# Kernel optimization log

Measured on AMD Instinct MI355X. Metric: run time of the kernel, lower is better.

The kernel has to match this reference:

```python
import jax, jax.numpy as jnp
import numpy as np

MAT_MODE = [(0, 1), (0, 2), (1, 2)]
VEC_MODE = [2, 1, 0]


def _sample_plane(plane, gx, gy):
    """Bilinear grid_sample, align_corners=True, border clamp.
    plane: [C,H,W]; gx,gy in [-1,1], shape [N]; grid x->W, y->H. Returns [C,N]."""
    C, H, W = plane.shape
    ix = (gx + 1.0) * 0.5 * (W - 1)
    iy = (gy + 1.0) * 0.5 * (H - 1)
    ix0f = jnp.clip(jnp.floor(ix), 0, W - 1)
    iy0f = jnp.clip(jnp.floor(iy), 0, H - 1)
    ix0 = ix0f.astype(jnp.int32)
    iy0 = iy0f.astype(jnp.int32)
    ix1 = jnp.minimum(ix0 + 1, W - 1)
    iy1 = jnp.minimum(iy0 + 1, H - 1)
    wx = ix - ix0f  # [N]
    wy = iy - iy0f
    v00 = plane[:, iy0, ix0]  # [C,N]
    v01 = plane[:, iy0, ix1]
    v10 = plane[:, iy1, ix0]
    v11 = plane[:, iy1, ix1]
    top = v00 + wx * (v01 - v00)
    bot = v10 + wx * (v11 - v10)
    return top + wy * (bot - top)


def _sample_line(line, gz):
    """1D linear interp (grid_sample on [C,G,1] with grid (0,z)). line: [C,G]. Returns [C,N]."""
    C, G = line.shape
    iz = (gz + 1.0) * 0.5 * (G - 1)
    iz0f = jnp.clip(jnp.floor(iz), 0, G - 1)
    iz0 = iz0f.astype(jnp.int32)
    iz1 = jnp.minimum(iz0 + 1, G - 1)
    wz = iz - iz0f
    v0 = line[:, iz0]
    v1 = line[:, iz1]
    return v0 + wz * (v1 - v0)


def setup_inputs() -> dict:
    key = jax.random.key(0)
    ks = jax.random.split(key, 7)
    N, C, G = 524288, 48, 512
    scale = 0.1 ** 0.5
    xyz = jax.random.uniform(ks[0], (N, 3), dtype=jnp.float32, minval=-1.0, maxval=1.0)
    planes = [scale * jax.random.normal(ks[1 + i], (C, G, G), dtype=jnp.float32) for i in range(3)]
    lines = [scale * jax.random.normal(ks[4 + i], (C, G), dtype=jnp.float32) for i in range(3)]
    return {"xyz": xyz,
            "plane0": planes[0], "plane1": planes[1], "plane2": planes[2],
            "line0": lines[0], "line1": lines[1], "line2": lines[2]}


def reference(xyz, plane0, plane1, plane2, line0, line1, line2):
    planes = (plane0, plane1, plane2)
    lines = (line0, line1, line2)
    feats = []
    for i in range(3):
        m0, m1 = MAT_MODE[i]
        pc = _sample_plane(planes[i], xyz[:, m0], xyz[:, m1])   # [C,N]
        lc = _sample_line(lines[i], xyz[:, VEC_MODE[i]])          # [C,N]
        feats.append(pc * lc)
    return tuple(feats)
```

## Files before the change

kernel.cpp:

```cpp
#include <hip/hip_runtime.h>
#include <hip/hip_fp16.h>

#define GSZ 512
#define CCH 48
#define GG (GSZ*GSZ)

__global__ __launch_bounds__(256) void transpose_plane(const float* __restrict__ in,
                                                       __half* __restrict__ out) {
    __shared__ float tile[CCH][65];
    const int t = threadIdx.x;
    const int pos0 = blockIdx.x * 64;
    #pragma unroll
    for (int k = 0; k < 12; ++k) {
        int e = k * 256 + t;
        int c = e >> 6;
        int p = e & 63;
        tile[c][p] = in[c * GG + pos0 + p];
    }
    __syncthreads();
    #pragma unroll
    for (int k = 0; k < 6; ++k) {
        int e = (k * 256 + t) * 2;
        int p = e / 48;
        int c = e - p * 48;
        __half2 h;
        h.x = __float2half(tile[c][p]);
        h.y = __float2half(tile[c + 1][p]);
        *((__half2*)(out + (size_t)pos0 * CCH + e)) = h;
    }
}

__global__ __launch_bounds__(256) void transpose_lines(
    const float* __restrict__ i0, const float* __restrict__ i1, const float* __restrict__ i2,
    __half* __restrict__ o0, __half* __restrict__ o1, __half* __restrict__ o2) {
    int idx = blockIdx.x * blockDim.x + threadIdx.x;
    const int total = CCH * GSZ;
    if (idx >= 3 * total) return;
    int w = idx / total;
    int r = idx - w * total;
    int c = r / GSZ;
    int p = r - c * GSZ;
    const float* in = (w == 0) ? i0 : (w == 1) ? i1 : i2;
    __half* out = (w == 0) ? o0 : (w == 1) ? o1 : o2;
    out[p * CCH + c] = __float2half(in[c * GSZ + p]);
}

union H8 { int4 v; __half h[8]; };

__global__ __launch_bounds__(256) void gather_fused(
    const float* __restrict__ xyz,
    const __half* __restrict__ p0, const __half* __restrict__ p1, const __half* __restrict__ p2,
    const __half* __restrict__ l0, const __half* __restrict__ l1, const __half* __restrict__ l2,
    float* __restrict__ out, int N) {
    int n = blockIdx.x * blockDim.x + threadIdx.x;
    if (n >= N) return;
    float x = xyz[3 * n + 0], y = xyz[3 * n + 1], z = xyz[3 * n + 2];

    float gx[3] = {x, x, y};
    float gy[3] = {y, z, z};
    float gz[3] = {z, y, x};

    int   po[3][4];
    int   lo[3][2];
    float wx[3], wy[3], wz[3];
    #pragma unroll
    for (int i = 0; i < 3; ++i) {
        float ix = (gx[i] + 1.0f) * 0.5f * (float)(GSZ - 1);
        float iy = (gy[i] + 1.0f) * 0.5f * (float)(GSZ - 1);
        float ix0f = fminf(fmaxf(floorf(ix), 0.0f), (float)(GSZ - 1));
        float iy0f = fminf(fmaxf(floorf(iy), 0.0f), (float)(GSZ - 1));
        int ix0 = (int)ix0f, iy0 = (int)iy0f;
        int ix1 = min(ix0 + 1, GSZ - 1);
        int iy1 = min(iy0 + 1, GSZ - 1);
        wx[i] = ix - ix0f;
        wy[i] = iy - iy0f;
        po[i][0] = (iy0 * GSZ + ix0) * CCH;
        po[i][1] = (iy0 * GSZ + ix1) * CCH;
        po[i][2] = (iy1 * GSZ + ix0) * CCH;
        po[i][3] = (iy1 * GSZ + ix1) * CCH;
        float iz = (gz[i] + 1.0f) * 0.5f * (float)(GSZ - 1);
        float iz0f = fminf(fmaxf(floorf(iz), 0.0f), (float)(GSZ - 1));
        int iz0 = (int)iz0f;
        int iz1 = min(iz0 + 1, GSZ - 1);
        wz[i] = iz - iz0f;
        lo[i][0] = iz0 * CCH;
        lo[i][1] = iz1 * CCH;
    }

    const size_t CN = (size_t)CCH * (size_t)N;
    #pragma unroll
    for (int i = 0; i < 3; ++i) {
        const __half* pp = (i == 0) ? p0 : (i == 1) ? p1 : p2;
        const __half* ll = (i == 0) ? l0 : (i == 1) ? l1 : l2;
        float* op = out + (size_t)i * CN + n;
        #pragma unroll
        for (int cc = 0; cc < CCH; cc += 8) {
            H8 a00, a01, a10, a11, b0, b1;
            a00.v = *(const int4*)(pp + po[i][0] + cc);
            a01.v = *(const int4*)(pp + po[i][1] + cc);
            a10.v = *(const int4*)(pp + po[i][2] + cc);
            a11.v = *(const int4*)(pp + po[i][3] + cc);
            b0.v  = *(const int4*)(ll + lo[i][0] + cc);
            b1.v  = *(const int4*)(ll + lo[i][1] + cc);
            #pragma unroll
            for (int j = 0; j < 8; ++j) {
                float v00 = __half2float(a00.h[j]);
                float v01 = __half2float(a01.h[j]);
                float v10 = __half2float(a10.h[j]);
                float v11 = __half2float(a11.h[j]);
                float top = fmaf(wx[i], v01 - v00, v00);
                float bot = fmaf(wx[i], v11 - v10, v10);
                float pc  = fmaf(wy[i], bot - top, top);
                float lv0 = __half2float(b0.h[j]);
                float lv1 = __half2float(b1.h[j]);
                float lc  = fmaf(wz[i], lv1 - lv0, lv0);
                op[(size_t)(cc + j) * N] = pc * lc;
            }
        }
    }
}

__global__ __launch_bounds__(256) void gather_direct(
    const float* __restrict__ xyz,
    const float* __restrict__ p0, const float* __restrict__ p1, const float* __restrict__ p2,
    const float* __restrict__ l0, const float* __restrict__ l1, const float* __restrict__ l2,
    float* __restrict__ out, int N) {
    int n = blockIdx.x * blockDim.x + threadIdx.x;
    if (n >= N) return;
    float x = xyz[3 * n + 0], y = xyz[3 * n + 1], z = xyz[3 * n + 2];
    float gx[3] = {x, x, y};
    float gy[3] = {y, z, z};
    float gz[3] = {z, y, x};
    int q[3][4], lz[3][2];
    float wx[3], wy[3], wz[3];
    #pragma unroll
    for (int i = 0; i < 3; ++i) {
        float ix = (gx[i] + 1.0f) * 0.5f * (float)(GSZ - 1);
        float iy = (gy[i] + 1.0f) * 0.5f * (float)(GSZ - 1);
        float ix0f = fminf(fmaxf(floorf(ix), 0.0f), (float)(GSZ - 1));
        float iy0f = fminf(fmaxf(floorf(iy), 0.0f), (float)(GSZ - 1));
        int ix0 = (int)ix0f, iy0 = (int)iy0f;
        int ix1 = min(ix0 + 1, GSZ - 1);
        int iy1 = min(iy0 + 1, GSZ - 1);
        wx[i] = ix - ix0f;
        wy[i] = iy - iy0f;
        q[i][0] = iy0 * GSZ + ix0;
        q[i][1] = iy0 * GSZ + ix1;
        q[i][2] = iy1 * GSZ + ix0;
        q[i][3] = iy1 * GSZ + ix1;
        float iz = (gz[i] + 1.0f) * 0.5f * (float)(GSZ - 1);
        float iz0f = fminf(fmaxf(floorf(iz), 0.0f), (float)(GSZ - 1));
        int iz0 = (int)iz0f;
        int iz1 = min(iz0 + 1, GSZ - 1);
        wz[i] = iz - iz0f;
        lz[i][0] = iz0;
        lz[i][1] = iz1;
    }
    const size_t CN = (size_t)CCH * (size_t)N;
    for (int c = 0; c < CCH; ++c) {
        #pragma unroll
        for (int i = 0; i < 3; ++i) {
            const float* pp = (i == 0) ? p0 : (i == 1) ? p1 : p2;
            const float* ll = (i == 0) ? l0 : (i == 1) ? l1 : l2;
            const float* pc_ = pp + (size_t)c * GG;
            float v00 = pc_[q[i][0]];
            float v01 = pc_[q[i][1]];
            float v10 = pc_[q[i][2]];
            float v11 = pc_[q[i][3]];
            float top = fmaf(wx[i], v01 - v00, v00);
            float bot = fmaf(wx[i], v11 - v10, v10);
            float pcv = fmaf(wy[i], bot - top, top);
            float lv0 = ll[c * GSZ + lz[i][0]];
            float lv1 = ll[c * GSZ + lz[i][1]];
            float lc  = fmaf(wz[i], lv1 - lv0, lv0);
            out[(size_t)i * CN + (size_t)c * N + n] = pcv * lc;
        }
    }
}

extern "C" void kernel_launch(void* const* d_in, const int* in_sizes, int n_in,
                              void* d_out, int out_size, void* d_ws, size_t ws_size,
                              hipStream_t stream) {
    const float* xyz = (const float*)d_in[0];
    const float* pl0 = (const float*)d_in[1];
    const float* pl1 = (const float*)d_in[2];
    const float* pl2 = (const float*)d_in[3];
    const float* ln0 = (const float*)d_in[4];
    const float* ln1 = (const float*)d_in[5];
    const float* ln2 = (const float*)d_in[6];
    float* out = (float*)d_out;
    const int N = in_sizes[0] / 3;

    const size_t planeElems = (size_t)GG * CCH;
    const size_t lineElems  = (size_t)GSZ * CCH;
    const size_t need = (3 * planeElems + 3 * lineElems) * sizeof(__half);

    if (ws_size >= need) {
        __half* wp0 = (__half*)d_ws;
        __half* wp1 = wp0 + planeElems;
        __half* wp2 = wp1 + planeElems;
        __half* wl0 = wp2 + planeElems;
        __half* wl1 = wl0 + lineElems;
        __half* wl2 = wl1 + lineElems;

        transpose_plane<<<GG / 64, 256, 0, stream>>>(pl0, wp0);
        transpose_plane<<<GG / 64, 256, 0, stream>>>(pl1, wp1);
        transpose_plane<<<GG / 64, 256, 0, stream>>>(pl2, wp2);
        transpose_lines<<<(3 * CCH * GSZ + 255) / 256, 256, 0, stream>>>(
            ln0, ln1, ln2, wl0, wl1, wl2);
        gather_fused<<<(N + 255) / 256, 256, 0, stream>>>(
            xyz, wp0, wp1, wp2, wl0, wl1, wl2, out, N);
    } else {
        gather_direct<<<(N + 255) / 256, 256, 0, stream>>>(
            xyz, pl0, pl1, pl2, ln0, ln1, ln2, out, N);
    }
}
```

Measured before the change: 941.1 us.

## Morton-sort query points before gathering to improve plane cache locality

Adds a counting sort of query points into a 32^3 Morton-ordered grid (histogram, single-block scan, atomic scatter). The gather then runs on the sorted points so neighbouring threads hit nearby plane texels, and writes fp16 features into a point-major buffer. A separate permute kernel restores the original order and writes the fp32 channel-major output. The three plane transposes are also merged into one launch. This adds four kernels, a memset and an extra fp16 round-trip of the features, and it only runs when the workspace is large enough.

```diff
diff --git a/kernel.cpp b/kernel.cpp
--- a/kernel.cpp
+++ b/kernel.cpp
@@ -4,9 +4,15 @@
 #define GSZ 512
 #define CCH 48
 #define GG (GSZ*GSZ)
-
-__global__ __launch_bounds__(256) void transpose_plane(const float* __restrict__ in,
-                                                       __half* __restrict__ out) {
+#define CBITS 5
+#define CDIM (1 << CBITS)
+#define CELLS (CDIM * CDIM * CDIM)
+
+__global__ __launch_bounds__(256) void transpose_planes3(
+    const float* __restrict__ i0, const float* __restrict__ i1, const float* __restrict__ i2,
+    __half* __restrict__ o0, __half* __restrict__ o1, __half* __restrict__ o2) {
+    const float* in = (blockIdx.y == 0) ? i0 : (blockIdx.y == 1) ? i1 : i2;
+    __half* out     = (blockIdx.y == 0) ? o0 : (blockIdx.y == 1) ? o1 : o2;
     __shared__ float tile[CCH][65];
     const int t = threadIdx.x;
     const int pos0 = blockIdx.x * 64;
@@ -45,23 +51,83 @@
     out[p * CCH + c] = __float2half(in[c * GSZ + p]);
 }
 
+__device__ __forceinline__ unsigned spread5(unsigned a) {
+    a &= 31u;
+    a = (a | (a << 8)) & 0x100Fu;
+    a = (a | (a << 4)) & 0x10C3u;
+    a = (a | (a << 2)) & 0x1249u;
+    return a;
+}
+__device__ __forceinline__ unsigned cell_of(float x, float y, float z) {
+    const float s = 0.5f * (float)CDIM;
+    unsigned cx = (unsigned)fminf(fmaxf((x + 1.0f) * s, 0.0f), (float)(CDIM - 1));
+    unsigned cy = (unsigned)fminf(fmaxf((y + 1.0f) * s, 0.0f), (float)(CDIM - 1));
+    unsigned cz = (unsigned)fminf(fmaxf((z + 1.0f) * s, 0.0f), (float)(CDIM - 1));
+    return spread5(cx) | (spread5(cy) << 1) | (spread5(cz) << 2);
+}
+
+__global__ __launch_bounds__(256) void hist_k(const float* __restrict__ xyz,
+                                              unsigned* __restrict__ hist, int N) {
+    int n = blockIdx.x * 256 + threadIdx.x;
+    if (n >= N) return;
+    float x = xyz[3 * n], y = xyz[3 * n + 1], z = xyz[3 * n + 2];
+    atomicAdd(&hist[cell_of(x, y, z)], 1u);
+}
+
+__global__ __launch_bounds__(1024) void scan_k(unsigned* __restrict__ h) {
+    __shared__ unsigned partials[1024];
+    const int t = threadIdx.x;
+    unsigned loc[CELLS / 1024];
+    unsigned s = 0;
+    #pragma unroll
+    for (int j = 0; j < CELLS / 1024; ++j) { loc[j] = h[t * (CELLS / 1024) + j]; s += loc[j]; }
+    partials[t] = s;
+    __syncthreads();
+    for (int off = 1; off < 1024; off <<= 1) {
+        unsigned v = (t >= off) ? partials[t - off] : 0u;
+        __syncthreads();
+        partials[t] += v;
+        __syncthreads();
+    }
+    unsigned running = (t > 0) ? partials[t - 1] : 0u;
+    #pragma unroll
+    for (int j = 0; j < CELLS / 1024; ++j) {
+        unsigned c = loc[j];
+        h[t * (CELLS / 1024) + j] = running;
+        running += c;
+    }
+}
+
+__global__ __launch_bounds__(256) void scatter_k(const float* __restrict__ xyz,
+                                                 unsigned* __restrict__ offs,
+                                                 unsigned* __restrict__ invPerm,
+                                                 float4* __restrict__ sxyz, int N) {
+    int n = blockIdx.x * 256 + threadIdx.x;
+    if (n >= N) return;
+    float x = xyz[3 * n], y = xyz[3 * n + 1], z = xyz[3 * n + 2];
+    unsigned p = atomicAdd(&offs[cell_of(x, y, z)], 1u);
+    invPerm[n] = p;
+    sxyz[p] = make_float4(x, y, z, 0.0f);
+}
+
 union H8 { int4 v; __half h[8]; };
 
-__global__ __launch_bounds__(256) void gather_fused(
-    const float* __restrict__ xyz,
+__global__ __launch_bounds__(256) void gather_sorted(
+    const float4* __restrict__ sxyz,
     const __half* __restrict__ p0, const __half* __restrict__ p1, const __half* __restrict__ p2,
     const __half* __restrict__ l0, const __half* __restrict__ l1, const __half* __restrict__ l2,
-    float* __restrict__ out, int N) {
-    int n = blockIdx.x * blockDim.x + threadIdx.x;
-    if (n >= N) return;
-    float x = xyz[3 * n + 0], y = xyz[3 * n + 1], z = xyz[3 * n + 2];
+    __half* __restrict__ feats, int N) {
+    int b = blockIdx.x, nb = gridDim.x;
+    int chunk = ((nb & 7) == 0) ? ((b & 7) * (nb >> 3) + (b >> 3)) : b;
+    int p = chunk * 256 + threadIdx.x;
+    if (p >= N) return;
+    float4 q = sxyz[p];
+    float x = q.x, y = q.y, z = q.z;
 
     float gx[3] = {x, x, y};
     float gy[3] = {y, z, z};
     float gz[3] = {z, y, x};
-
-    int   po[3][4];
-    int   lo[3][2];
+    int po[3][4], lo[3][2];
     float wx[3], wy[3], wz[3];
     #pragma unroll
     for (int i = 0; i < 3; ++i) {
@@ -87,6 +153,96 @@
         lo[i][1] = iz1 * CCH;
     }
 
+    __half* fb = feats + (size_t)p * 144;
+    #pragma unroll
+    for (int i = 0; i < 3; ++i) {
+        const __half* pp = (i == 0) ? p0 : (i == 1) ? p1 : p2;
+        const __half* ll = (i == 0) ? l0 : (i == 1) ? l1 : l2;
+        #pragma unroll
+        for (int cc = 0; cc < CCH; cc += 8) {
+            H8 a00, a01, a10, a11, b0, b1, r;
+            a00.v = *(const int4*)(pp + po[i][0] + cc);
+            a01.v = *(const int4*)(pp + po[i][1] + cc);
+            a10.v = *(const int4*)(pp + po[i][2] + cc);
+            a11.v = *(const int4*)(pp + po[i][3] + cc);
+            b0.v  = *(const int4*)(ll + lo[i][0] + cc);
+            b1.v  = *(const int4*)(ll + lo[i][1] + cc);
+            #pragma unroll
+            for (int j = 0; j < 8; ++j) {
+                float v00 = __half2float(a00.h[j]);
+                float v01 = __half2float(a01.h[j]);
+                float v10 = __half2float(a10.h[j]);
+                float v11 = __half2float(a11.h[j]);
+                float top = fmaf(wx[i], v01 - v00, v00);
+                float bot = fmaf(wx[i], v11 - v10, v10);
+                float pc  = fmaf(wy[i], bot - top, top);
+                float lv0 = __half2float(b0.h[j]);
+                float lv1 = __half2float(b1.h[j]);
+                float lc  = fmaf(wz[i], lv1 - lv0, lv0);
+                r.h[j] = __float2half(pc * lc);
+            }
+            *(int4*)(fb + i * 48 + cc) = r.v;
+        }
+    }
+}
+
+__global__ __launch_bounds__(256) void permute_k(
+    const unsigned* __restrict__ invPerm, const __half* __restrict__ feats,
+    float* __restrict__ out, int N) {
+    int n = blockIdx.x * 256 + threadIdx.x;
+    if (n >= N) return;
+    const __half* fb = feats + (size_t)invPerm[n] * 144;
+    const size_t CN = (size_t)CCH * (size_t)N;
+    #pragma unroll
+    for (int i = 0; i < 3; ++i) {
+        H8 v[6];
+        #pragma unroll
+        for (int k = 0; k < 6; ++k) v[k].v = *(const int4*)(fb + i * 48 + k * 8);
+        float* op = out + (size_t)i * CN + n;
+        #pragma unroll
+        for (int k = 0; k < 6; ++k)
+            #pragma unroll
+            for (int j = 0; j < 8; ++j)
+                op[(size_t)(k * 8 + j) * N] = __half2float(v[k].h[j]);
+    }
+}
+
+__global__ __launch_bounds__(256) void gather_fused(
+    const float* __restrict__ xyz,
+    const __half* __restrict__ p0, const __half* __restrict__ p1, const __half* __restrict__ p2,
+    const __half* __restrict__ l0, const __half* __restrict__ l1, const __half* __restrict__ l2,
+    float* __restrict__ out, int N) {
+    int n = blockIdx.x * 256 + threadIdx.x;
+    if (n >= N) return;
+    float x = xyz[3 * n], y = xyz[3 * n + 1], z = xyz[3 * n + 2];
+    float gx[3] = {x, x, y};
+    float gy[3] = {y, z, z};
+    float gz[3] = {z, y, x};
+    int po[3][4], lo[3][2];
+    float wx[3], wy[3], wz[3];
+    #pragma unroll
+    for (int i = 0; i < 3; ++i) {
+        float ix = (gx[i] + 1.0f) * 0.5f * (float)(GSZ - 1);
+        float iy = (gy[i] + 1.0f) * 0.5f * (float)(GSZ - 1);
+        float ix0f = fminf(fmaxf(floorf(ix), 0.0f), (float)(GSZ - 1));
+        float iy0f = fminf(fmaxf(floorf(iy), 0.0f), (float)(GSZ - 1));
+        int ix0 = (int)ix0f, iy0 = (int)iy0f;
+        int ix1 = min(ix0 + 1, GSZ - 1);
+        int iy1 = min(iy0 + 1, GSZ - 1);
+        wx[i] = ix - ix0f;
+        wy[i] = iy - iy0f;
+        po[i][0] = (iy0 * GSZ + ix0) * CCH;
+        po[i][1] = (iy0 * GSZ + ix1) * CCH;
+        po[i][2] = (iy1 * GSZ + ix0) * CCH;
+        po[i][3] = (iy1 * GSZ + ix1) * CCH;
+        float iz = (gz[i] + 1.0f) * 0.5f * (float)(GSZ - 1);
+        float iz0f = fminf(fmaxf(floorf(iz), 0.0f), (float)(GSZ - 1));
+        int iz0 = (int)iz0f;
+        int iz1 = min(iz0 + 1, GSZ - 1);
+        wz[i] = iz - iz0f;
+        lo[i][0] = iz0 * CCH;
+        lo[i][1] = iz1 * CCH;
+    }
     const size_t CN = (size_t)CCH * (size_t)N;
     #pragma unroll
     for (int i = 0; i < 3; ++i) {
@@ -125,9 +281,9 @@
     const float* __restrict__ p0, const float* __restrict__ p1, const float* __restrict__ p2,
     const float* __restrict__ l0, const float* __restrict__ l1, const float* __restrict__ l2,
     float* __restrict__ out, int N) {
-    int n = blockIdx.x * blockDim.x + threadIdx.x;
+    int n = blockIdx.x * 256 + threadIdx.x;
     if (n >= N) return;
-    float x = xyz[3 * n + 0], y = xyz[3 * n + 1], z = xyz[3 * n + 2];
+    float x = xyz[3 * n], y = xyz[3 * n + 1], z = xyz[3 * n + 2];
     float gx[3] = {x, x, y};
     float gy[3] = {y, z, z};
     float gz[3] = {z, y, x};
@@ -193,25 +349,53 @@
 
     const size_t planeElems = (size_t)GG * CCH;
     const size_t lineElems  = (size_t)GSZ * CCH;
-    const size_t need = (3 * planeElems + 3 * lineElems) * sizeof(__half);
-
-    if (ws_size >= need) {
-        __half* wp0 = (__half*)d_ws;
+
+    auto align256 = [](size_t v) { return (v + 255) & ~(size_t)255; };
+    size_t off = 0;
+    size_t o_planes = off; off = align256(off + 3 * planeElems * sizeof(__half));
+    size_t o_lines  = off; off = align256(off + 3 * lineElems * sizeof(__half));
+    size_t o_hist   = off; off = align256(off + (size_t)CELLS * sizeof(unsigned));
+    size_t o_iperm  = off; off = align256(off + (size_t)N * sizeof(unsigned));
+    size_t o_sxyz   = off; off = align256(off + (size_t)N * sizeof(float4));
+    size_t o_feats  = off; off = align256(off + (size_t)N * 144 * sizeof(__half));
+    const size_t need_sort = off;
+    const size_t need_old  = align256(3 * planeElems * sizeof(__half)) +
+                             align256(3 * lineElems * sizeof(__half));
+
+    char* ws = (char*)d_ws;
+    const int nblk = (N + 255) / 256;
+
+    if (ws_size >= need_sort) {
+        __half* wp0 = (__half*)(ws + o_planes);
         __half* wp1 = wp0 + planeElems;
         __half* wp2 = wp1 + planeElems;
-        __half* wl0 = wp2 + planeElems;
+        __half* wl0 = (__half*)(ws + o_lines);
         __half* wl1 = wl0 + lineElems;
         __half* wl2 = wl1 + lineElems;
-
-        transpose_plane<<<GG / 64, 256, 0, stream>>>(pl0, wp0);
-        transpose_plane<<<GG / 64, 256, 0, stream>>>(pl1, wp1);
-        transpose_plane<<<GG / 64, 256, 0, stream>>>(pl2, wp2);
-        transpose_lines<<<(3 * CCH * GSZ + 255) / 256, 256, 0, stream>>>(
-            ln0, ln1, ln2, wl0, wl1, wl2);
-        gather_fused<<<(N + 255) / 256, 256, 0, stream>>>(
-            xyz, wp0, wp1, wp2, wl0, wl1, wl2, out, N);
+        unsigned* hist  = (unsigned*)(ws + o_hist);
+        unsigned* iperm = (unsigned*)(ws + o_iperm);
+        float4*   sxyz  = (float4*)(ws + o_sxyz);
+        __half*   feats = (__half*)(ws + o_feats);
+
+        transpose_planes3<<<dim3(GG / 64, 3), 256, 0, stream>>>(pl0, pl1, pl2, wp0, wp1, wp2);
+        transpose_lines<<<(3 * CCH * GSZ + 255) / 256, 256, 0, stream>>>(ln0, ln1, ln2, wl0, wl1, wl2);
+        hipMemsetAsync(hist, 0, (size_t)CELLS * sizeof(unsigned), stream);
+        hist_k<<<nblk, 256, 0, stream>>>(xyz, hist, N);
+        scan_k<<<1, 1024, 0, stream>>>(hist);
+        scatter_k<<<nblk, 256, 0, stream>>>(xyz, hist, iperm, sxyz, N);
+        gather_sorted<<<nblk, 256, 0, stream>>>(sxyz, wp0, wp1, wp2, wl0, wl1, wl2, feats, N);
+        permute_k<<<nblk, 256, 0, stream>>>(iperm, feats, out, N);
+    } else if (ws_size >= need_old) {
+        __half* wp0 = (__half*)(ws + o_planes);
+        __half* wp1 = wp0 + planeElems;
+        __half* wp2 = wp1 + planeElems;
+        __half* wl0 = (__half*)(ws + o_lines);
+        __half* wl1 = wl0 + lineElems;
+        __half* wl2 = wl1 + lineElems;
+        transpose_planes3<<<dim3(GG / 64, 3), 256, 0, stream>>>(pl0, pl1, pl2, wp0, wp1, wp2);
+        transpose_lines<<<(3 * CCH * GSZ + 255) / 256, 256, 0, stream>>>(ln0, ln1, ln2, wl0, wl1, wl2);
+        gather_fused<<<nblk, 256, 0, stream>>>(xyz, wp0, wp1, wp2, wl0, wl1, wl2, out, N);
     } else {
-        gather_direct<<<(N + 255) / 256, 256, 0, stream>>>(
-            xyz, pl0, pl1, pl2, ln0, ln1, ln2, out, N);
-    }
-}
+        gather_direct<<<nblk, 256, 0, stream>>>(xyz, pl0, pl1, pl2, ln0, ln1, ln2, out, N);
+    }
+}
```

New measurement: 885.1 us. -5.9%, faster.
